# Kernel tuning notes

Measured on AMD Instinct MI355X. Metric: run time of the kernel, lower is better.

The kernel has to match this reference:

```python
import jax, jax.numpy as jnp
import numpy as np
import math

B, S, E_PHI, E_F, H_F, N_HEADS = 2, 2048, 1024, 1024, 1024, 16


def setup_inputs() -> dict:
    key = jax.random.key(0)
    ks = jax.random.split(key, 7)
    return {
        "q": jax.random.normal(ks[0], (B, S, E_PHI), dtype=jnp.float32),
        "k": jax.random.normal(ks[1], (B, S, E_PHI), dtype=jnp.float32),
        "v": jax.random.normal(ks[2], (B, S, E_F), dtype=jnp.float32),
        # weights stored as [in, out]; applied as x @ W (same math as nn.Linear with W^T)
        "W_q": jax.random.normal(ks[3], (E_PHI, H_F), dtype=jnp.float32) * 0.02,
        "W_k": jax.random.normal(ks[4], (E_PHI, H_F), dtype=jnp.float32) * 0.02,
        "W_v": jax.random.normal(ks[5], (E_F, H_F), dtype=jnp.float32) * 0.02,
        "W_o": jax.random.normal(ks[6], (H_F, E_F), dtype=jnp.float32) * 0.02,
    }


def reference(q, k, v, W_q, W_k, W_v, W_o):
    Bq, Sq, _ = q.shape
    Dh = H_F // N_HEADS
    scale = 1.0 / math.sqrt(H_F)
    # projections -> [B, H, S, Dh]
    qh = (q @ W_q).reshape(Bq, Sq, N_HEADS, Dh).transpose(0, 2, 1, 3)
    kh = (k @ W_k).reshape(Bq, Sq, N_HEADS, Dh).transpose(0, 2, 1, 3)
    vh = (v @ W_v).reshape(Bq, Sq, N_HEADS, Dh).transpose(0, 2, 1, 3)
    # near-causal mask: mask out j >= i (triu incl. diagonal), EXCEPT position [0,0]
    mask = jnp.triu(jnp.ones((Sq, Sq), dtype=bool), 0).at[0, 0].set(False)
    scores = jnp.einsum('bhsd,bhtd->bhst', qh, kh) * scale  # [B,H,S,S]
    scores = jnp.where(mask, -jnp.inf, scores)
    probs = jax.nn.softmax(scores, axis=-1)  # dropout = identity (eval mode)
    out = jnp.einsum('bhst,bhtd->bhsd', probs, vh)  # [B,H,S,Dh]
    out = out.transpose(0, 2, 1, 3).reshape(Bq, Sq, H_F)
    return out @ W_o
```

## Files before the change

kernel.cpp:

```cpp
#include <hip/hip_runtime.h>
#include <type_traits>

#define S_LEN 2048
#define NHEAD 16
#define DHEAD 64
#define EMB   1024
#define NBATCH 2

typedef __bf16 bf16_t;
typedef bf16_t bf16x8 __attribute__((ext_vector_type(8)));
typedef float  f32x4  __attribute__((ext_vector_type(4)));
typedef unsigned short us_t;
typedef us_t   us8    __attribute__((ext_vector_type(8)));
typedef us_t   us4    __attribute__((ext_vector_type(4)));
typedef unsigned int u32x4 __attribute__((ext_vector_type(4)));
typedef unsigned int u32x2 __attribute__((ext_vector_type(2)));
typedef short  s16x4  __attribute__((ext_vector_type(4)));

static __device__ __forceinline__ bf16x8 ld_bf16x8(const us_t* p) {
  return __builtin_bit_cast(bf16x8, *reinterpret_cast<const us8*>(p));
}
static __device__ __forceinline__ us_t f2bf(float f) {
  bf16_t h = (bf16_t)f;
  return __builtin_bit_cast(us_t, h);
}
static __device__ __forceinline__ unsigned cvt_pk_bf16(float lo, float hi) {
  unsigned r;
  asm("v_cvt_pk_bf16_f32 %0, %1, %2" : "=v"(r) : "v"(lo), "v"(hi));
  return r;
}
#if __has_builtin(__builtin_amdgcn_exp2f)
#define EXP2(x) __builtin_amdgcn_exp2f(x)
#else
#define EXP2(x) exp2f(x)
#endif
static __device__ __forceinline__ void gload16(const void* g, void* lds) {
  __builtin_amdgcn_global_load_lds((const __attribute__((address_space(1))) void*)g,
                                   (__attribute__((address_space(3))) void*)lds,
                                   16, 0, 0);
}

__global__ __launch_bounds__(256) void prep(const float* __restrict__ q,
                                            const float* __restrict__ k,
                                            const float* __restrict__ v,
                                            const float* __restrict__ W0,
                                            const float* __restrict__ W1,
                                            const float* __restrict__ W2,
                                            const float* __restrict__ W3,
                                            us_t* __restrict__ Qb,
                                            us_t* __restrict__ Kb,
                                            us_t* __restrict__ Vb,
                                            us_t* __restrict__ T0,
                                            us_t* __restrict__ T1,
                                            us_t* __restrict__ T2,
                                            us_t* __restrict__ T3) {
  const int z = blockIdx.z;
  if (z < 3) {
    const float* A = (z == 0) ? q : (z == 1) ? k : v;
    us_t* O = (z == 0) ? Qb : (z == 1) ? Kb : Vb;
    const int flat = blockIdx.y * 32 + blockIdx.x;
    const size_t i = ((size_t)flat * 256 + threadIdx.x) * 8;
    f32x4 lo = *reinterpret_cast<const f32x4*>(A + i);
    f32x4 hi = *reinterpret_cast<const f32x4*>(A + i + 4);
    us8 w;
#pragma unroll
    for (int j = 0; j < 4; ++j) { w[j] = f2bf(lo[j]); w[j + 4] = f2bf(hi[j]); }
    *reinterpret_cast<us8*>(O + i) = w;
  } else {
    if (blockIdx.y >= EMB / 32) return;
    __shared__ float tile[32][33];
    const int zz = z - 3;
    const float* W = (zz == 0) ? W0 : (zz == 1) ? W1 : (zz == 2) ? W2 : W3;
    us_t* WT = (zz == 0) ? T0 : (zz == 1) ? T1 : (zz == 2) ? T2 : T3;
    const int n0 = blockIdx.x * 32, k0 = blockIdx.y * 32;
    const int tx = threadIdx.x & 31, ty = threadIdx.x >> 5;
#pragma unroll
    for (int i = 0; i < 32; i += 8)
      tile[ty + i][tx] = W[(size_t)(k0 + ty + i) * EMB + n0 + tx];
    __syncthreads();
#pragma unroll
    for (int i = 0; i < 32; i += 8)
      WT[(size_t)(n0 + ty + i) * EMB + k0 + tx] = f2bf(tile[tx][ty + i]);
  }
}

template<int MODE>
static __device__ __forceinline__ void gemm_core(const us_t* __restrict__ A,
                                                 const us_t* __restrict__ BT,
                                                 void* __restrict__ O,
                                                 int mt, int nt,
                                                 char (*As)[8192], char (*Bs)[8192]) {
  const int lane = threadIdx.x & 63;
  const int wave = threadIdx.x >> 6;
  const int wm = (wave >> 1) * 64;
  const int wn = (wave & 1) * 64;
  const int lr = lane & 15;
  const int lg = lane >> 4;

  f32x4 acc[4][4] = {};

  auto stage = [&](int buf, int k0) {
#pragma unroll
    for (int i = 0; i < 2; ++i) {
      const int seg = wave * 2 + i;
      const int r = seg * 16 + (lane >> 2);
      const int cb = (lane & 3) * 16;
      gload16((const char*)A + ((size_t)(mt * 128 + r) * EMB + k0) * 2 + cb,
              &As[buf][seg * 1024]);
      gload16((const char*)BT + ((size_t)(nt * 128 + r) * EMB + k0) * 2 + cb,
              &Bs[buf][seg * 1024]);
    }
  };

  stage(0, 0);
  __syncthreads();

  for (int ks = 0; ks < EMB / 32; ++ks) {
    const int cur = ks & 1;
    if (ks + 1 < EMB / 32) stage(cur ^ 1, (ks + 1) * 32);
    bf16x8 af[4], bfr[4];
#pragma unroll
    for (int i = 0; i < 4; ++i)
      af[i] = ld_bf16x8((const us_t*)&As[cur][(wm + 16 * i + lr) * 64 + lg * 16]);
#pragma unroll
    for (int j = 0; j < 4; ++j)
      bfr[j] = ld_bf16x8((const us_t*)&Bs[cur][(wn + 16 * j + lr) * 64 + lg * 16]);
#pragma unroll
    for (int i = 0; i < 4; ++i)
#pragma unroll
      for (int j = 0; j < 4; ++j)
        acc[i][j] = __builtin_amdgcn_mfma_f32_16x16x32_bf16(af[i], bfr[j], acc[i][j], 0, 0, 0);
    __syncthreads();
  }

  const int crow = (lane >> 4) * 4;
#pragma unroll
  for (int i = 0; i < 4; ++i)
#pragma unroll
    for (int j = 0; j < 4; ++j)
#pragma unroll
      for (int r = 0; r < 4; ++r) {
        const int m = mt * 128 + wm + 16 * i + crow + r;
        const int n = nt * 128 + wn + 16 * j + lr;
        const float val = acc[i][j][r];
        if constexpr (MODE == 2) {
          ((float*)O)[(size_t)m * EMB + n] = val;
        } else {
          us_t* o = (us_t*)O;
          const int b = m >> 11, s = m & (S_LEN - 1);
          const int h = n >> 6, d = n & 63;
          if constexpr (MODE == 0)
            o[(((size_t)(b * NHEAD + h) * S_LEN + s) << 6) + d] = f2bf(val);
          else
            o[((size_t)(b * NHEAD + h) * DHEAD + d) * S_LEN + s] = f2bf(val);
        }
      }
}

__global__ __launch_bounds__(256) void proj3(const us_t* __restrict__ A0,
                                             const us_t* __restrict__ A1,
                                             const us_t* __restrict__ A2,
                                             const us_t* __restrict__ B0,
                                             const us_t* __restrict__ B1,
                                             const us_t* __restrict__ B2,
                                             us_t* __restrict__ O0,
                                             us_t* __restrict__ O1,
                                             us_t* __restrict__ O2) {
  __shared__ char As[2][8192];
  __shared__ char Bs[2][8192];
  const int f = blockIdx.x;
  const int w = (f & 7) * 96 + (f >> 3);
  const int z = w >> 8;
  const int rem = w & 255;
  const int mt = rem >> 3, nt = rem & 7;
  const us_t* A = (z == 0) ? A0 : (z == 1) ? A1 : A2;
  const us_t* BT = (z == 0) ? B0 : (z == 1) ? B1 : B2;
  us_t* O = (z == 0) ? O0 : (z == 1) ? O1 : O2;
  if (z < 2)
    gemm_core<0>(A, BT, O, mt, nt, As, Bs);
  else
    gemm_core<1>(A, BT, O, mt, nt, As, Bs);
}

__global__ __launch_bounds__(256) void gemmout(const us_t* __restrict__ A,
                                               const us_t* __restrict__ BT,
                                               float* __restrict__ O) {
  __shared__ char As[2][8192];
  __shared__ char Bs[2][8192];
  const int f = blockIdx.x;
  const int w = (f & 7) * 32 + (f >> 3);
  const int mt = w >> 3, nt = w & 7;
  gemm_core<2>(A, BT, O, mt, nt, As, Bs);
}

__global__ __launch_bounds__(256, 4) void attn64(const us_t* __restrict__ Qh,
                                                 const us_t* __restrict__ Kh,
                                                 const us_t* __restrict__ Vt,
                                                 us_t* __restrict__ AO) {
  __shared__ char Ks[2][8192];
  __shared__ char Vs[2][8192];
  const int flat = blockIdx.y * 32 + blockIdx.x;
  const int bh = (flat & 7) * 4 + ((flat >> 3) & 3);
  const int qt = 31 - (flat >> 5);
  const int lane = threadIdx.x & 63;
  const int wave = threadIdx.x >> 6;
  const int lr = lane & 15;
  const int lg = lane >> 4;
  const int q_glob = qt * 64 + wave * 16 + lr;

  const us_t* qbase = Qh + ((size_t)bh * S_LEN + q_glob) * DHEAD;
  bf16x8 qf[2] = { ld_bf16x8(qbase + lg * 8), ld_bf16x8(qbase + 32 + lg * 8) };

  const us_t* kbase0 = Kh + (size_t)bh * S_LEN * DHEAD;
  const us_t* vbase0 = Vt + (size_t)bh * DHEAD * S_LEN;

  int koff[8];
#pragma unroll
  for (int ks = 0; ks < 2; ++ks)
#pragma unroll
    for (int j = 0; j < 4; ++j)
      koff[ks * 4 + j] = (16 * j + lr) * 128 + ((ks * 64 + lg * 16) ^ ((lr & 7) << 4));
  int voff[16];
#pragma unroll
  for (int jk = 0; jk < 4; ++jk)
#pragma unroll
    for (int jd = 0; jd < 4; ++jd)
      voff[jk * 4 + jd] = (16 * jd + lr) * 128 + ((32 * jk + 8 * lg) ^ ((lr & 7) << 4));

  auto stage = [&](int buf, int t0) {
#pragma unroll
    for (int i = 0; i < 2; ++i) {
      const int seg = wave * 2 + i;
      const int r = seg * 8 + (lane >> 3);
      const int c16 = (lane & 7) ^ (lane >> 3);
      gload16(kbase0 + (size_t)(t0 + r) * DHEAD + c16 * 8, &Ks[buf][seg * 1024]);
      gload16(vbase0 + (size_t)r * S_LEN + t0 + c16 * 8, &Vs[buf][seg * 1024]);
    }
  };

  f32x4 oaccT[4] = {};
  float mrow = -1e9f;
  float lsum = 0.f;
  const float c = 0.045084220f;

  stage(0, 0);
  __syncthreads();

  for (int tt = 0; tt <= qt; ++tt) {
    const int cur = tt & 1;
    if (tt < qt) stage(cur ^ 1, (tt + 1) * 64);

    f32x4 sc[4] = {};
    __builtin_amdgcn_s_setprio(1);
#pragma unroll
    for (int ks = 0; ks < 2; ++ks)
#pragma unroll
      for (int j = 0; j < 4; ++j) {
        bf16x8 ak = ld_bf16x8((const us_t*)&Ks[cur][koff[ks * 4 + j]]);
        sc[j] = __builtin_amdgcn_mfma_f32_16x16x32_bf16(ak, qf[ks], sc[j], 0, 0, 0);
      }
    __builtin_amdgcn_s_setprio(0);

    if (tt == qt) {
#pragma unroll
      for (int j = 0; j < 4; ++j)
#pragma unroll
        for (int r = 0; r < 4; ++r) {
          const int t_g = tt * 64 + 16 * j + 4 * lg + r;
          if (!((t_g < q_glob) || (q_glob == 0 && t_g == 0))) sc[j][r] = -1e30f;
        }
    }

    float mx = sc[0][0];
#pragma unroll
    for (int j = 0; j < 4; ++j)
#pragma unroll
      for (int r = 0; r < 4; ++r) mx = fmaxf(mx, sc[j][r]);
    const float mxc = mx * c;
    if (__any(mxc > mrow + 8.f)) {
      float mc = mxc;
      mc = fmaxf(mc, __shfl_xor(mc, 16, 64));
      mc = fmaxf(mc, __shfl_xor(mc, 32, 64));
      const float m2 = fmaxf(mrow, mc);
      const float alpha = EXP2(mrow - m2);
      lsum *= alpha;
#pragma unroll
      for (int j = 0; j < 4; ++j)
#pragma unroll
        for (int r = 0; r < 4; ++r) oaccT[j][r] *= alpha;
      mrow = m2;
    }

    unsigned int pk[4][2];
    float ps = 0.f;
#pragma unroll
    for (int j = 0; j < 4; ++j) {
      float p0 = EXP2(__builtin_fmaf(sc[j][0], c, -mrow));
      float p1 = EXP2(__builtin_fmaf(sc[j][1], c, -mrow));
      float p2 = EXP2(__builtin_fmaf(sc[j][2], c, -mrow));
      float p3 = EXP2(__builtin_fmaf(sc[j][3], c, -mrow));
      ps += (p0 + p1) + (p2 + p3);
      pk[j][0] = cvt_pk_bf16(p0, p1);
      pk[j][1] = cvt_pk_bf16(p2, p3);
    }
    lsum += ps;

    __builtin_amdgcn_s_setprio(1);
#pragma unroll
    for (int jk = 0; jk < 4; ++jk) {
      s16x4 pf = __builtin_bit_cast(s16x4, (u32x2){pk[jk][0], pk[jk][1]});
#pragma unroll
      for (int jd = 0; jd < 4; ++jd) {
        s16x4 av = __builtin_bit_cast(s16x4,
            *reinterpret_cast<const us4*>(&Vs[cur][voff[jk * 4 + jd]]));
        oaccT[jd] = __builtin_amdgcn_mfma_f32_16x16x16bf16_1k(av, pf, oaccT[jd], 0, 0, 0);
      }
    }
    __builtin_amdgcn_s_setprio(0);
    __syncthreads();
  }

  lsum += __shfl_xor(lsum, 16, 64);
  lsum += __shfl_xor(lsum, 32, 64);
  const float inv = 1.0f / lsum;
  const int b = bh >> 4, h = bh & 15;
  us_t* aout = AO + (size_t)(b * S_LEN + q_glob) * EMB + h * DHEAD;
#pragma unroll
  for (int j = 0; j < 4; ++j) {
    us4 w;
#pragma unroll
    for (int r = 0; r < 4; ++r) w[r] = f2bf(oaccT[j][r] * inv);
    *reinterpret_cast<us4*>(aout + 16 * j + 4 * lg) = w;
  }
}

extern "C" void kernel_launch(void* const* d_in, const int* in_sizes, int n_in,
                              void* d_out, int out_size, void* d_ws, size_t ws_size,
                              hipStream_t stream) {
  const float* q  = (const float*)d_in[0];
  const float* k  = (const float*)d_in[1];
  const float* v  = (const float*)d_in[2];
  const float* Wq = (const float*)d_in[3];
  const float* Wk = (const float*)d_in[4];
  const float* Wv = (const float*)d_in[5];
  const float* Wo = (const float*)d_in[6];
  float* out = (float*)d_out;

  char* ws = (char*)d_ws;
  const size_t MB = 1024 * 1024;
  us_t* WqT = (us_t*)(ws + 0 * MB);
  us_t* WkT = (us_t*)(ws + 2 * MB);
  us_t* WvT = (us_t*)(ws + 4 * MB);
  us_t* WoT = (us_t*)(ws + 6 * MB);
  us_t* Qh  = (us_t*)(ws + 8 * MB);
  us_t* Kh  = (us_t*)(ws + 16 * MB);
  us_t* Vt  = (us_t*)(ws + 24 * MB);
  us_t* AO  = (us_t*)(ws + 32 * MB);
  us_t* Qb  = (us_t*)(ws + 32 * MB);
  us_t* Kb  = (us_t*)(ws + 40 * MB);
  us_t* Vb  = (us_t*)(ws + 48 * MB);

  prep<<<dim3(32, 64, 7), 256, 0, stream>>>(q, k, v, Wq, Wk, Wv, Wo,
                                            Qb, Kb, Vb, WqT, WkT, WvT, WoT);

  proj3<<<768, 256, 0, stream>>>(Qb, Kb, Vb, WqT, WkT, WvT, Qh, Kh, Vt);

  attn64<<<dim3(S_LEN / 64, NBATCH * NHEAD), 256, 0, stream>>>(Qh, Kh, Vt, AO);

  gemmout<<<256, 256, 0, stream>>>(AO, WoT, out);
}
```

Baseline: 130.6 us.

## Enlarge attention query tile to 128 rows with two query chunks per wave

Each attention block now covers 128 query rows instead of 64, and each wave handles two 16-row query chunks that share every K/V fragment read from LDS. This halves K/V global staging traffic per query and doubles MFMA work per LDS load. In exchange the grid shrinks to 512 blocks, occupancy drops to 2 blocks per CU, and register pressure rises. Causal load imbalance also becomes coarser, and waves 0-1 sit idle on the final tile.

```diff
diff --git a/kernel.cpp b/kernel.cpp
--- a/kernel.cpp
+++ b/kernel.cpp
@@ -193,23 +193,26 @@
   gemm_core<2>(A, BT, O, mt, nt, As, Bs);
 }
 
-__global__ __launch_bounds__(256, 4) void attn64(const us_t* __restrict__ Qh,
-                                                 const us_t* __restrict__ Kh,
-                                                 const us_t* __restrict__ Vt,
-                                                 us_t* __restrict__ AO) {
+__global__ __launch_bounds__(256, 2) void attn128(const us_t* __restrict__ Qh,
+                                                  const us_t* __restrict__ Kh,
+                                                  const us_t* __restrict__ Vt,
+                                                  us_t* __restrict__ AO) {
   __shared__ char Ks[2][8192];
   __shared__ char Vs[2][8192];
   const int flat = blockIdx.y * 32 + blockIdx.x;
   const int bh = (flat & 7) * 4 + ((flat >> 3) & 3);
-  const int qt = 31 - (flat >> 5);
+  const int qt = 15 - (flat >> 5);
   const int lane = threadIdx.x & 63;
   const int wave = threadIdx.x >> 6;
   const int lr = lane & 15;
   const int lg = lane >> 4;
-  const int q_glob = qt * 64 + wave * 16 + lr;
-
-  const us_t* qbase = Qh + ((size_t)bh * S_LEN + q_glob) * DHEAD;
-  bf16x8 qf[2] = { ld_bf16x8(qbase + lg * 8), ld_bf16x8(qbase + 32 + lg * 8) };
+  const int qw = qt * 128 + wave * 32;
+  const int qg[2] = { qw + lr, qw + 16 + lr };
+
+  const us_t* qb0 = Qh + ((size_t)bh * S_LEN + qg[0]) * DHEAD;
+  const us_t* qb1 = Qh + ((size_t)bh * S_LEN + qg[1]) * DHEAD;
+  bf16x8 qf[2][2] = { { ld_bf16x8(qb0 + lg * 8), ld_bf16x8(qb0 + 32 + lg * 8) },
+                      { ld_bf16x8(qb1 + lg * 8), ld_bf16x8(qb1 + 32 + lg * 8) } };
 
   const us_t* kbase0 = Kh + (size_t)bh * S_LEN * DHEAD;
   const us_t* vbase0 = Vt + (size_t)bh * DHEAD * S_LEN;
@@ -238,99 +241,114 @@
     }
   };
 
-  f32x4 oaccT[4] = {};
-  float mrow = -1e9f;
-  float lsum = 0.f;
+  f32x4 oaccT[2][4] = {};
+  float mrow[2] = { -1e9f, -1e9f };
+  float lsum[2] = { 0.f, 0.f };
   const float c = 0.045084220f;
 
   stage(0, 0);
   __syncthreads();
 
-  for (int tt = 0; tt <= qt; ++tt) {
+  const int NT = 2 * qt + 2;
+  for (int tt = 0; tt < NT; ++tt) {
     const int cur = tt & 1;
-    if (tt < qt) stage(cur ^ 1, (tt + 1) * 64);
-
-    f32x4 sc[4] = {};
-    __builtin_amdgcn_s_setprio(1);
-#pragma unroll
-    for (int ks = 0; ks < 2; ++ks)
-#pragma unroll
-      for (int j = 0; j < 4; ++j) {
-        bf16x8 ak = ld_bf16x8((const us_t*)&Ks[cur][koff[ks * 4 + j]]);
-        sc[j] = __builtin_amdgcn_mfma_f32_16x16x32_bf16(ak, qf[ks], sc[j], 0, 0, 0);
+    if (tt + 1 < NT) stage(cur ^ 1, (tt + 1) * 64);
+    const bool skip = (wave < 2) && (tt == NT - 1);
+    if (!skip) {
+      f32x4 sc[2][4] = {};
+      __builtin_amdgcn_s_setprio(1);
+#pragma unroll
+      for (int ks = 0; ks < 2; ++ks)
+#pragma unroll
+        for (int j = 0; j < 4; ++j) {
+          bf16x8 ak = ld_bf16x8((const us_t*)&Ks[cur][koff[ks * 4 + j]]);
+          sc[0][j] = __builtin_amdgcn_mfma_f32_16x16x32_bf16(ak, qf[0][ks], sc[0][j], 0, 0, 0);
+          sc[1][j] = __builtin_amdgcn_mfma_f32_16x16x32_bf16(ak, qf[1][ks], sc[1][j], 0, 0, 0);
+        }
+      __builtin_amdgcn_s_setprio(0);
+
+      if (tt * 64 + 63 >= qw) {
+#pragma unroll
+        for (int qc = 0; qc < 2; ++qc)
+#pragma unroll
+          for (int j = 0; j < 4; ++j)
+#pragma unroll
+            for (int r = 0; r < 4; ++r) {
+              const int t_g = tt * 64 + 16 * j + 4 * lg + r;
+              const int qq = qg[qc];
+              if (!((t_g < qq) || (qq == 0 && t_g == 0))) sc[qc][j][r] = -1e30f;
+            }
       }
-    __builtin_amdgcn_s_setprio(0);
-
-    if (tt == qt) {
-#pragma unroll
-      for (int j = 0; j < 4; ++j)
-#pragma unroll
-        for (int r = 0; r < 4; ++r) {
-          const int t_g = tt * 64 + 16 * j + 4 * lg + r;
-          if (!((t_g < q_glob) || (q_glob == 0 && t_g == 0))) sc[j][r] = -1e30f;
-        }
+
+      unsigned int pk[2][4][2];
+#pragma unroll
+      for (int qc = 0; qc < 2; ++qc) {
+        float mx = sc[qc][0][0];
+#pragma unroll
+        for (int j = 0; j < 4; ++j)
+#pragma unroll
+          for (int r = 0; r < 4; ++r) mx = fmaxf(mx, sc[qc][j][r]);
+        const float mxc = mx * c;
+        if (__any(mxc > mrow[qc] + 8.f)) {
+          float mc = mxc;
+          mc = fmaxf(mc, __shfl_xor(mc, 16, 64));
+          mc = fmaxf(mc, __shfl_xor(mc, 32, 64));
+          const float m2 = fmaxf(mrow[qc], mc);
+          const float alpha = EXP2(mrow[qc] - m2);
+          lsum[qc] *= alpha;
+#pragma unroll
+          for (int j = 0; j < 4; ++j)
+#pragma unroll
+            for (int r = 0; r < 4; ++r) oaccT[qc][j][r] *= alpha;
+          mrow[qc] = m2;
+        }
+        float ps = 0.f;
+#pragma unroll
+        for (int j = 0; j < 4; ++j) {
+          float p0 = EXP2(__builtin_fmaf(sc[qc][j][0], c, -mrow[qc]));
+          float p1 = EXP2(__builtin_fmaf(sc[qc][j][1], c, -mrow[qc]));
+          float p2 = EXP2(__builtin_fmaf(sc[qc][j][2], c, -mrow[qc]));
+          float p3 = EXP2(__builtin_fmaf(sc[qc][j][3], c, -mrow[qc]));
+          ps += (p0 + p1) + (p2 + p3);
+          pk[qc][j][0] = cvt_pk_bf16(p0, p1);
+          pk[qc][j][1] = cvt_pk_bf16(p2, p3);
+        }
+        lsum[qc] += ps;
+      }
+
+      __builtin_amdgcn_s_setprio(1);
+#pragma unroll
+      for (int jk = 0; jk < 4; ++jk) {
+        s16x4 pf0 = __builtin_bit_cast(s16x4, (u32x2){pk[0][jk][0], pk[0][jk][1]});
+        s16x4 pf1 = __builtin_bit_cast(s16x4, (u32x2){pk[1][jk][0], pk[1][jk][1]});
+#pragma unroll
+        for (int jd = 0; jd < 4; ++jd) {
+          s16x4 av = __builtin_bit_cast(s16x4,
+              *reinterpret_cast<const us4*>(&Vs[cur][voff[jk * 4 + jd]]));
+          oaccT[0][jd] = __builtin_amdgcn_mfma_f32_16x16x16bf16_1k(av, pf0, oaccT[0][jd], 0, 0, 0);
+          oaccT[1][jd] = __builtin_amdgcn_mfma_f32_16x16x16bf16_1k(av, pf1, oaccT[1][jd], 0, 0, 0);
+        }
+      }
+      __builtin_amdgcn_s_setprio(0);
     }
-
-    float mx = sc[0][0];
-#pragma unroll
-    for (int j = 0; j < 4; ++j)
-#pragma unroll
-      for (int r = 0; r < 4; ++r) mx = fmaxf(mx, sc[j][r]);
-    const float mxc = mx * c;
-    if (__any(mxc > mrow + 8.f)) {
-      float mc = mxc;
-      mc = fmaxf(mc, __shfl_xor(mc, 16, 64));
-      mc = fmaxf(mc, __shfl_xor(mc, 32, 64));
-      const float m2 = fmaxf(mrow, mc);
-      const float alpha = EXP2(mrow - m2);
-      lsum *= alpha;
-#pragma unroll
-      for (int j = 0; j < 4; ++j)
-#pragma unroll
-        for (int r = 0; r < 4; ++r) oaccT[j][r] *= alpha;
-      mrow = m2;
-    }
-
-    unsigned int pk[4][2];
-    float ps = 0.f;
-#pragma unroll
-    for (int j = 0; j < 4; ++j) {
-      float p0 = EXP2(__builtin_fmaf(sc[j][0], c, -mrow));
-      float p1 = EXP2(__builtin_fmaf(sc[j][1], c, -mrow));
-      float p2 = EXP2(__builtin_fmaf(sc[j][2], c, -mrow));
-      float p3 = EXP2(__builtin_fmaf(sc[j][3], c, -mrow));
-      ps += (p0 + p1) + (p2 + p3);
-      pk[j][0] = cvt_pk_bf16(p0, p1);
-      pk[j][1] = cvt_pk_bf16(p2, p3);
-    }
-    lsum += ps;
-
-    __builtin_amdgcn_s_setprio(1);
-#pragma unroll
-    for (int jk = 0; jk < 4; ++jk) {
-      s16x4 pf = __builtin_bit_cast(s16x4, (u32x2){pk[jk][0], pk[jk][1]});
-#pragma unroll
-      for (int jd = 0; jd < 4; ++jd) {
-        s16x4 av = __builtin_bit_cast(s16x4,
-            *reinterpret_cast<const us4*>(&Vs[cur][voff[jk * 4 + jd]]));
-        oaccT[jd] = __builtin_amdgcn_mfma_f32_16x16x16bf16_1k(av, pf, oaccT[jd], 0, 0, 0);
-      }
-    }
-    __builtin_amdgcn_s_setprio(0);
     __syncthreads();
   }
 
-  lsum += __shfl_xor(lsum, 16, 64);
-  lsum += __shfl_xor(lsum, 32, 64);
-  const float inv = 1.0f / lsum;
   const int b = bh >> 4, h = bh & 15;
-  us_t* aout = AO + (size_t)(b * S_LEN + q_glob) * EMB + h * DHEAD;
-#pragma unroll
-  for (int j = 0; j < 4; ++j) {
-    us4 w;
-#pragma unroll
-    for (int r = 0; r < 4; ++r) w[r] = f2bf(oaccT[j][r] * inv);
-    *reinterpret_cast<us4*>(aout + 16 * j + 4 * lg) = w;
+#pragma unroll
+  for (int qc = 0; qc < 2; ++qc) {
+    float ls = lsum[qc];
+    ls += __shfl_xor(ls, 16, 64);
+    ls += __shfl_xor(ls, 32, 64);
+    const float inv = 1.0f / ls;
+    us_t* aout = AO + (size_t)(b * S_LEN + qg[qc]) * EMB + h * DHEAD;
+#pragma unroll
+    for (int j = 0; j < 4; ++j) {
+      us4 w;
+#pragma unroll
+      for (int r = 0; r < 4; ++r) w[r] = f2bf(oaccT[qc][j][r] * inv);
+      *reinterpret_cast<us4*>(aout + 16 * j + 4 * lg) = w;
+    }
   }
 }
 
@@ -365,7 +383,7 @@
 
   proj3<<<768, 256, 0, stream>>>(Qb, Kb, Vb, WqT, WkT, WvT, Qh, Kh, Vt);
 
-  attn64<<<dim3(S_LEN / 64, NBATCH * NHEAD), 256, 0, stream>>>(Qh, Kh, Vt, AO);
+  attn128<<<dim3(32, 16), 256, 0, stream>>>(Qh, Kh, Vt, AO);
 
   gemmout<<<256, 256, 0, stream>>>(AO, WoT, out);
 }
```

Result: slower. 139.4 us (+6.8%).

## Fuse fp32-to-bf16 activation conversion into projection GEMM and rebalance attention tile order

Applied to the files above, without the earlier changes.

Drops the separate pass that converted q/k/v activations to bf16. The projection GEMM now reads fp32 rows directly, converts them with packed cvt instructions, and writes bf16 into LDS itself. This removes a full write and re-read of 24MB of bf16 intermediates, at the cost of synchronous register-path loads in place of async global_load_lds for the A operand. Separately, the attention kernel's query-tile ordering is changed to interleave heavy and light causal tiles across block groups, to even out load.

```diff
diff --git a/kernel.cpp b/kernel.cpp
--- a/kernel.cpp
+++ b/kernel.cpp
@@ -40,52 +40,31 @@
                                    16, 0, 0);
 }
 
-__global__ __launch_bounds__(256) void prep(const float* __restrict__ q,
-                                            const float* __restrict__ k,
-                                            const float* __restrict__ v,
-                                            const float* __restrict__ W0,
+__global__ __launch_bounds__(256) void prep(const float* __restrict__ W0,
                                             const float* __restrict__ W1,
                                             const float* __restrict__ W2,
                                             const float* __restrict__ W3,
-                                            us_t* __restrict__ Qb,
-                                            us_t* __restrict__ Kb,
-                                            us_t* __restrict__ Vb,
                                             us_t* __restrict__ T0,
                                             us_t* __restrict__ T1,
                                             us_t* __restrict__ T2,
                                             us_t* __restrict__ T3) {
+  __shared__ float tile[32][33];
   const int z = blockIdx.z;
-  if (z < 3) {
-    const float* A = (z == 0) ? q : (z == 1) ? k : v;
-    us_t* O = (z == 0) ? Qb : (z == 1) ? Kb : Vb;
-    const int flat = blockIdx.y * 32 + blockIdx.x;
-    const size_t i = ((size_t)flat * 256 + threadIdx.x) * 8;
-    f32x4 lo = *reinterpret_cast<const f32x4*>(A + i);
-    f32x4 hi = *reinterpret_cast<const f32x4*>(A + i + 4);
-    us8 w;
-#pragma unroll
-    for (int j = 0; j < 4; ++j) { w[j] = f2bf(lo[j]); w[j + 4] = f2bf(hi[j]); }
-    *reinterpret_cast<us8*>(O + i) = w;
-  } else {
-    if (blockIdx.y >= EMB / 32) return;
-    __shared__ float tile[32][33];
-    const int zz = z - 3;
-    const float* W = (zz == 0) ? W0 : (zz == 1) ? W1 : (zz == 2) ? W2 : W3;
-    us_t* WT = (zz == 0) ? T0 : (zz == 1) ? T1 : (zz == 2) ? T2 : T3;
-    const int n0 = blockIdx.x * 32, k0 = blockIdx.y * 32;
-    const int tx = threadIdx.x & 31, ty = threadIdx.x >> 5;
-#pragma unroll
-    for (int i = 0; i < 32; i += 8)
-      tile[ty + i][tx] = W[(size_t)(k0 + ty + i) * EMB + n0 + tx];
-    __syncthreads();
-#pragma unroll
-    for (int i = 0; i < 32; i += 8)
-      WT[(size_t)(n0 + ty + i) * EMB + k0 + tx] = f2bf(tile[tx][ty + i]);
-  }
-}
-
-template<int MODE>
-static __device__ __forceinline__ void gemm_core(const us_t* __restrict__ A,
+  const float* W = (z == 0) ? W0 : (z == 1) ? W1 : (z == 2) ? W2 : W3;
+  us_t* WT = (z == 0) ? T0 : (z == 1) ? T1 : (z == 2) ? T2 : T3;
+  const int n0 = blockIdx.x * 32, k0 = blockIdx.y * 32;
+  const int tx = threadIdx.x & 31, ty = threadIdx.x >> 5;
+#pragma unroll
+  for (int i = 0; i < 32; i += 8)
+    tile[ty + i][tx] = W[(size_t)(k0 + ty + i) * EMB + n0 + tx];
+  __syncthreads();
+#pragma unroll
+  for (int i = 0; i < 32; i += 8)
+    WT[(size_t)(n0 + ty + i) * EMB + k0 + tx] = f2bf(tile[tx][ty + i]);
+}
+
+template<int MODE, bool AF32>
+static __device__ __forceinline__ void gemm_core(const void* __restrict__ Ap,
                                                  const us_t* __restrict__ BT,
                                                  void* __restrict__ O,
                                                  int mt, int nt,
@@ -104,10 +83,18 @@
     for (int i = 0; i < 2; ++i) {
       const int seg = wave * 2 + i;
       const int r = seg * 16 + (lane >> 2);
-      const int cb = (lane & 3) * 16;
-      gload16((const char*)A + ((size_t)(mt * 128 + r) * EMB + k0) * 2 + cb,
-              &As[buf][seg * 1024]);
-      gload16((const char*)BT + ((size_t)(nt * 128 + r) * EMB + k0) * 2 + cb,
+      if constexpr (AF32) {
+        const float* ap = (const float*)Ap + (size_t)(mt * 128 + r) * EMB + k0 + (lane & 3) * 8;
+        f32x4 lo = *reinterpret_cast<const f32x4*>(ap);
+        f32x4 hi = *reinterpret_cast<const f32x4*>(ap + 4);
+        u32x4 w = { cvt_pk_bf16(lo[0], lo[1]), cvt_pk_bf16(lo[2], lo[3]),
+                    cvt_pk_bf16(hi[0], hi[1]), cvt_pk_bf16(hi[2], hi[3]) };
+        *reinterpret_cast<u32x4*>(&As[buf][seg * 1024 + lane * 16]) = w;
+      } else {
+        gload16((const char*)Ap + ((size_t)(mt * 128 + r) * EMB + k0) * 2 + (lane & 3) * 16,
+                &As[buf][seg * 1024]);
+      }
+      gload16((const char*)BT + ((size_t)(nt * 128 + r) * EMB + k0) * 2 + (lane & 3) * 16,
               &Bs[buf][seg * 1024]);
     }
   };
@@ -157,9 +144,9 @@
       }
 }
 
-__global__ __launch_bounds__(256) void proj3(const us_t* __restrict__ A0,
-                                             const us_t* __restrict__ A1,
-                                             const us_t* __restrict__ A2,
+__global__ __launch_bounds__(256) void proj3(const float* __restrict__ A0,
+                                             const float* __restrict__ A1,
+                                             const float* __restrict__ A2,
                                              const us_t* __restrict__ B0,
                                              const us_t* __restrict__ B1,
                                              const us_t* __restrict__ B2,
@@ -173,13 +160,13 @@
   const int z = w >> 8;
   const int rem = w & 255;
   const int mt = rem >> 3, nt = rem & 7;
-  const us_t* A = (z == 0) ? A0 : (z == 1) ? A1 : A2;
+  const float* A = (z == 0) ? A0 : (z == 1) ? A1 : A2;
   const us_t* BT = (z == 0) ? B0 : (z == 1) ? B1 : B2;
   us_t* O = (z == 0) ? O0 : (z == 1) ? O1 : O2;
   if (z < 2)
-    gemm_core<0>(A, BT, O, mt, nt, As, Bs);
+    gemm_core<0, true>(A, BT, O, mt, nt, As, Bs);
   else
-    gemm_core<1>(A, BT, O, mt, nt, As, Bs);
+    gemm_core<1, true>(A, BT, O, mt, nt, As, Bs);
 }
 
 __global__ __launch_bounds__(256) void gemmout(const us_t* __restrict__ A,
@@ -190,7 +177,7 @@
   const int f = blockIdx.x;
   const int w = (f & 7) * 32 + (f >> 3);
   const int mt = w >> 3, nt = w & 7;
-  gemm_core<2>(A, BT, O, mt, nt, As, Bs);
+  gemm_core<2, false>(A, BT, O, mt, nt, As, Bs);
 }
 
 __global__ __launch_bounds__(256, 4) void attn64(const us_t* __restrict__ Qh,
@@ -201,7 +188,9 @@
   __shared__ char Vs[2][8192];
   const int flat = blockIdx.y * 32 + blockIdx.x;
   const int bh = (flat & 7) * 4 + ((flat >> 3) & 3);
-  const int qt = 31 - (flat >> 5);
+  const int g = flat >> 5;
+  const int Q = g >> 3, p = g & 7;
+  const int qt = (Q == 0) ? 31 - p : (Q == 1) ? 16 + p : (Q == 2) ? 15 - p : p;
   const int lane = threadIdx.x & 63;
   const int wave = threadIdx.x >> 6;
   const int lr = lane & 15;
@@ -356,16 +345,12 @@
   us_t* Kh  = (us_t*)(ws + 16 * MB);
   us_t* Vt  = (us_t*)(ws + 24 * MB);
   us_t* AO  = (us_t*)(ws + 32 * MB);
-  us_t* Qb  = (us_t*)(ws + 32 * MB);
-  us_t* Kb  = (us_t*)(ws + 40 * MB);
-  us_t* Vb  = (us_t*)(ws + 48 * MB);
-
-  prep<<<dim3(32, 64, 7), 256, 0, stream>>>(q, k, v, Wq, Wk, Wv, Wo,
-                                            Qb, Kb, Vb, WqT, WkT, WvT, WoT);
-
-  proj3<<<768, 256, 0, stream>>>(Qb, Kb, Vb, WqT, WkT, WvT, Qh, Kh, Vt);
-
-  attn64<<<dim3(S_LEN / 64, NBATCH * NHEAD), 256, 0, stream>>>(Qh, Kh, Vt, AO);
+
+  prep<<<dim3(32, 32, 4), 256, 0, stream>>>(Wq, Wk, Wv, Wo, WqT, WkT, WvT, WoT);
+
+  proj3<<<768, 256, 0, stream>>>(q, k, v, WqT, WkT, WvT, Qh, Kh, Vt);
+
+  attn64<<<dim3(32, 32), 256, 0, stream>>>(Qh, Kh, Vt, AO);
 
   gemmout<<<256, 256, 0, stream>>>(AO, WoT, out);
 }
```

Result: faster. 126.4 us (-3.2%).
